# Optimization experiments

Hardware: AMD Instinct MI355X
Metric: run time of the kernel (lower is better)

## Reference

```python
import jax, jax.numpy as jnp
import numpy as np

# --- static mask-construction config (mirrors FlexAttnFunc.init_mask args) ---
B = 1
L_F, L_H, L_W = 8, 20, 36      # latent_shape[2:]
A_F, A_H, A_W = 8, 1, 1        # action_shape[2:]
PATCH = (1, 2, 2)
CHUNK = 1
PAD = 176
WINDOW = 6
DIM, HEADS, DHEAD = 1536, 12, 128
EPS = 1e-5


def _make_ids():
    lf, lh, lw = L_F // PATCH[0], L_H // PATCH[1], L_W // PATCH[2]
    lat_seq = np.repeat(np.arange(B), lf * lh * lw)
    act_seq = np.repeat(np.arange(B), A_F * A_H * A_W)
    seq = np.concatenate([lat_seq, lat_seq, act_seq, act_seq])
    lat_fr = np.broadcast_to(np.arange(L_F)[None, :, None, None], (B, L_F, lh, lw)).reshape(-1)
    act_fr = np.broadcast_to(np.arange(A_F)[None, :, None, None], (B, A_F, A_H, A_W)).reshape(-1)
    fr = np.concatenate([lat_fr // CHUNK * 2] * 2 + [act_fr // CHUNK * 2 + 1] * 2)
    nz = np.concatenate([np.zeros_like(lat_fr), np.ones_like(lat_fr),
                         np.zeros_like(act_fr), np.ones_like(act_fr)])
    pad = np.full(PAD, -1, dtype=np.int64)
    return (np.concatenate([seq, pad]).astype(np.int32),
            np.concatenate([fr, pad]).astype(np.int32),
            np.concatenate([nz, pad]).astype(np.int32))


def setup_inputs() -> dict:
    key = jax.random.key(0)
    ks = jax.random.split(key, 8)
    seq, fr, nz = _make_ids()
    S = seq.shape[0]  # 3072
    sd = 0.02
    return {
        'x': jax.random.normal(ks[0], (1, S, DIM), jnp.float32),
        'Wq': jax.random.normal(ks[1], (DIM, DIM), jnp.float32) * sd,
        'bq': jnp.zeros((DIM,), jnp.float32),
        'Wk': jax.random.normal(ks[2], (DIM, DIM), jnp.float32) * sd,
        'bk': jnp.zeros((DIM,), jnp.float32),
        'Wv': jax.random.normal(ks[3], (DIM, DIM), jnp.float32) * sd,
        'bv': jnp.zeros((DIM,), jnp.float32),
        'gq': 1.0 + jax.random.normal(ks[4], (DIM,), jnp.float32) * sd,
        'gk': 1.0 + jax.random.normal(ks[5], (DIM,), jnp.float32) * sd,
        'Wo': jax.random.normal(ks[6], (DIM, DIM), jnp.float32) * sd,
        'bo': jnp.zeros((DIM,), jnp.float32),
        'seq_ids': jnp.asarray(seq),
        'frame_ids': jnp.asarray(fr),
        'noise_ids': jnp.asarray(nz),
        'window_size': WINDOW,
    }


def _rms(u, g):
    # torch.nn.RMSNorm over last dim (size heads*dim_head), elementwise affine
    return u * jax.lax.rsqrt(jnp.mean(u * u, axis=-1, keepdims=True) + EPS) * g


def _mask(seq_ids, frame_ids, noise_ids, window_size):
    sq, sk = seq_ids[:, None], seq_ids[None, :]
    fq, fk = frame_ids[:, None], frame_ids[None, :]
    nq, nk = noise_ids[:, None], noise_ids[None, :]
    seq_ok = (sq == sk) & (sq >= 0) & (sk >= 0)
    c2c = (nq == 1) & (nk == 1) & (fk <= fq)      # clean->clean, block causal incl self
    n2c = (nq == 0) & (nk == 1) & (fk < fq)       # noise->clean, causal excl self
    n2n = (nq == 0) & (nk == 0) & (fk == fq)      # noise->noise, same frame only
    win = jnp.abs(fq - fk) <= window_size
    return (c2c | n2c | n2n) & seq_ok & win


def reference(x, Wq, bq, Wk, bk, Wv, bv, gq, gk, Wo, bo,
              seq_ids, frame_ids, noise_ids, window_size):
    S = x.shape[1]
    q = _rms(x @ Wq + bq, gq)[0].reshape(S, HEADS, DHEAD)
    k = _rms(x @ Wk + bk, gk)[0].reshape(S, HEADS, DHEAD)
    v = (x @ Wv + bv)[0].reshape(S, HEADS, DHEAD)
    mask = _mask(seq_ids, frame_ids, noise_ids, window_size)  # [S,S] bool
    scores = jnp.einsum('qhd,khd->hqk', q, k) * (DHEAD ** -0.5)
    scores = jnp.where(mask[None], scores, jnp.float32(-1e9))
    attn = jax.nn.softmax(scores, axis=-1)
    o = jnp.einsum('hqk,khd->qhd', attn, v)
    # zero out padded (fully-masked) query rows
    o = o * (seq_ids >= 0).astype(o.dtype)[:, None, None]
    y = o.reshape(1, S, HEADS * DHEAD) @ Wo + bo
    return y
```

## Files before the change

kernel.cpp:

```cpp
#include <hip/hip_runtime.h>
#include <hip/hip_bf16.h>
#include <stdint.h>

typedef __bf16 bf16x8 __attribute__((ext_vector_type(8)));
typedef float f32x4 __attribute__((ext_vector_type(4)));

__device__ __forceinline__ unsigned short f2bf(float f) {
  union { float f; unsigned int u; } v; v.f = f;
  unsigned int u = v.u;
  unsigned int r = (u + 0x7fffu + ((u >> 16) & 1u)) >> 16;
  return (unsigned short)r;
}
__device__ __forceinline__ float bf2f(unsigned short s) {
  union { unsigned int u; float f; } v; v.u = ((unsigned int)s) << 16; return v.f;
}

__global__ __launch_bounds__(256) void setup(
    const float* __restrict__ x,
    const float* __restrict__ Wq, const float* __restrict__ Wk,
    const float* __restrict__ Wv, const float* __restrict__ Wo,
    const int* __restrict__ seq, const int* __restrict__ fr,
    const int* __restrict__ nz, const int* __restrict__ wsz,
    unsigned short* __restrict__ x_bf, unsigned short* __restrict__ wt,
    unsigned long long* __restrict__ tbm, unsigned char* __restrict__ mb,
    float* __restrict__ ssq, int S) {
  __shared__ __align__(16) unsigned char smu[16384];
  int b = blockIdx.x, tid = threadIdx.x;
  if (b < 1152) {
    int base = b * 1024 + tid;
    for (int j = 0; j < 4; j++) {
      int i = base + j * 256;
      float4 v = ((const float4*)x)[i];
      ushort4 o;
      o.x = f2bf(v.x); o.y = f2bf(v.y); o.z = f2bf(v.z); o.w = f2bf(v.w);
      ((ushort4*)x_bf)[i] = o;
    }
  } else if (b < 3456) {
    int id = b - 1152;
    int z = id / 576, rem = id % 576;
    int kx = rem % 24, ny = rem / 24;
    const float* W = z == 0 ? Wq : (z == 1 ? Wk : (z == 2 ? Wv : Wo));
    unsigned short (*t)[65] = (unsigned short(*)[65])smu;
    int k0 = kx * 64, n0 = ny * 64;
    const int N = 1536, K = 1536;
    for (int i = 0; i < 16; i++) {
      int e = tid + i * 256;
      int r = e >> 6, c = e & 63;
      t[r][c] = f2bf(W[(size_t)(k0 + r) * N + n0 + c]);
    }
    __syncthreads();
    for (int i = 0; i < 16; i++) {
      int e = tid + i * 256;
      int r = e >> 6, c = e & 63;
      wt[(size_t)(z * 1536 + n0 + r) * K + k0 + c] = t[c][r];
    }
  } else if (b == 3456) {
    int* ks_ = (int*)smu;
    unsigned int* tm_ = (unsigned int*)(smu + 12288);
    int W = wsz[0];
    for (int i = tid; i < S; i += 256) {
      int sq = seq[i];
      ks_[i] = (sq < 0) ? 0 : ((1 << 9) | ((nz[i] & 1) << 8) | (fr[i] & 15) | (sq << 10));
    }
    for (int i = tid; i < 6144; i += 256) ssq[i] = 0.f;
    __syncthreads();
    for (int t = tid; t < S / 32; t += 256) {
      unsigned int m = 0;
      for (int j = 0; j < 32; j++) {
        int a = ks_[t * 32 + j];
        if (a & (1 << 9)) m |= (a & (1 << 8)) ? (1u << (16 + (a & 15))) : (1u << (a & 15));
      }
      tm_[t] = m;
    }
    __syncthreads();
    for (int qg = tid; qg < S / 16; qg += 256) {
      unsigned int allowed = 0;
      for (int j = 0; j < 16; j++) {
        int a = ks_[qg * 16 + j];
        if (!(a & (1 << 9))) continue;
        int fq = a & 15, nq = (a >> 8) & 1;
        int lo = fq - W; if (lo < 0) lo = 0;
        unsigned int lom = ~((1u << lo) - 1);
        if (nq) allowed |= (((1u << (fq + 1)) - 1) & lom) << 16;
        else    allowed |= ((((1u << fq) - 1) & lom) << 16) | (1u << fq);
      }
      unsigned long long b0 = 0, b1 = 0;
      for (int t = 0; t < 96; t++)
        if (tm_[t] & allowed) { if (t < 64) b0 |= 1ull << t; else b1 |= 1ull << (t - 64); }
      tbm[qg * 2] = b0; tbm[qg * 2 + 1] = b1;
    }
  } else {
    int qg = b - 3457;
    int* ks_ = (int*)smu;
    int W = wsz[0];
    for (int i = tid; i < S; i += 256) {
      int sq = seq[i];
      ks_[i] = (sq < 0) ? 0 : ((1 << 9) | ((nz[i] & 1) << 8) | (fr[i] & 15) | (sq << 10));
    }
    __syncthreads();
    int wave = tid >> 6, lane = tid & 63, quad = lane >> 4, l16 = lane & 15;
    int aq[4];
    for (int r = 0; r < 4; r++) aq[r] = ks_[qg * 16 + quad * 4 + r];
    for (int t = wave; t < 96; t += 4) {
      int ak[2] = { ks_[t * 32 + l16], ks_[t * 32 + 16 + l16] };
      unsigned int byte = 0;
      for (int nt = 0; nt < 2; nt++) {
        int a = ak[nt];
        int kfr = a & 15, knz = (a >> 8) & 1, kvb = (a >> 9) & 1, ksq = a >> 10;
        for (int r = 0; r < 4; r++) {
          int bq_ = aq[r];
          int qfr = bq_ & 15, qnz = (bq_ >> 8) & 1, qvb = (bq_ >> 9) & 1, qsq = bq_ >> 10;
          bool ok  = qvb && kvb && (qsq == ksq);
          bool c2c = qnz && knz && (kfr <= qfr);
          bool n2c = !qnz && knz && (kfr < qfr);
          bool n2n = !qnz && !knz && (kfr == qfr);
          int df = qfr - kfr; df = df < 0 ? -df : df;
          if ((c2c || n2c || n2n) && ok && (df <= W)) byte |= 1u << (nt * 4 + r);
        }
      }
      mb[((size_t)qg * 96 + t) * 64 + lane] = (unsigned char)byte;
    }
  }
}

__global__ __launch_bounds__(512) void gemm_qkv(
    const unsigned short* __restrict__ A, const unsigned short* __restrict__ Bt,
    const float* __restrict__ bq, const float* __restrict__ bk, const float* __restrict__ bv,
    const float* __restrict__ gq, const float* __restrict__ gk,
    unsigned short* __restrict__ qt, unsigned short* __restrict__ ktb,
    unsigned short* __restrict__ vtb, float* __restrict__ ssq, int S) {
  __shared__ __align__(16) unsigned short smem[65536];
  int tid = threadIdx.x, wid = tid >> 6, lane = tid & 63;
  int quad = lane >> 4, l16 = lane & 15;
  int m0 = blockIdx.x * 256, n0 = blockIdx.y * 256;
  int wm = (wid >> 2) * 128;
  int wn = (wid & 3) * 64;
  int lr = lane >> 3;
  int lsw = ((lane & 7) ^ lr) * 8;
  int sx = l16 & 7;

  f32x4 acc[8][4] = {};

#define STAGEQ(t_, q_) do { \
    if ((t_) < 24) { \
      int b_ = (t_) & 1; \
      int k0_ = (t_) * 64; \
      unsigned short* ldsb = ((q_) < 2) ? (smem + b_ * 16384) : (smem + 32768 + b_ * 16384); \
      const unsigned short* gsrc = ((q_) < 2) ? A : Bt; \
      int rbase = ((q_) < 2) ? m0 : n0; \
      int lo8_ = ((q_) & 1) * 8; \
      for (int c_ = 0; c_ < 2; c_++) { \
        int chunk = lo8_ + c_ * 16 + wid; \
        const unsigned short* src = gsrc + (size_t)(rbase + chunk * 8 + lr) * 1536 + k0_ + lsw; \
        __builtin_amdgcn_global_load_lds( \
            (const __attribute__((address_space(1))) unsigned int*)src, \
            (__attribute__((address_space(3))) unsigned int*)(ldsb + chunk * 512 + lane * 8), 16, 0, 0); \
      } \
    } } while (0)

  STAGEQ(0, 0); STAGEQ(0, 1); STAGEQ(0, 2); STAGEQ(0, 3);
  STAGEQ(1, 0);
  asm volatile("s_waitcnt vmcnt(2)" ::: "memory");
  __builtin_amdgcn_s_barrier();
  __builtin_amdgcn_sched_barrier(0);

#define PHASE(p) do { \
    constexpr int q_ = (p) & 3; \
    constexpr int tb_ = (p) >> 2; \
    constexpr int k8_ = (q_ >> 1) * 4; \
    constexpr int mi0_ = (q_ & 1) * 4; \
    unsigned short* Ab = smem + tb_ * 16384; \
    unsigned short* Bb = smem + 32768 + tb_ * 16384; \
    int so_ = ((k8_ + quad) ^ sx) << 3; \
    if constexpr ((q_ & 1) == 0) { \
      for (int nj = 0; nj < 4; nj++) \
        bfr[nj] = *(const bf16x8*)&Bb[(wn + nj * 16 + l16) * 64 + so_]; \
    } \
    bf16x8 af[4]; \
    for (int ii = 0; ii < 4; ii++) \
      af[ii] = *(const bf16x8*)&Ab[(wm + (mi0_ + ii) * 16 + l16) * 64 + so_]; \
    STAGEQ(2 * i + kStT[p], kStQ[p]); \
    __builtin_amdgcn_sched_barrier(0); \
    __builtin_amdgcn_s_barrier(); \
    asm volatile("s_waitcnt lgkmcnt(0)" ::: "memory"); \
    __builtin_amdgcn_sched_barrier(0); \
    __builtin_amdgcn_s_setprio(1); \
    for (int ii = 0; ii < 4; ii++) \
      for (int nj = 0; nj < 4; nj++) \
        acc[mi0_ + ii][nj] = __builtin_amdgcn_mfma_f32_16x16x32_bf16(af[ii], bfr[nj], acc[mi0_ + ii][nj], 0, 0, 0); \
    __builtin_amdgcn_s_setprio(0); \
    if constexpr (q_ == 3) { asm volatile("s_waitcnt vmcnt(2)" ::: "memory"); } \
    __builtin_amdgcn_s_barrier(); \
    __builtin_amdgcn_sched_barrier(0); \
  } while (0)

  constexpr int kStT[8] = {1, 1, 1, 2, 2, 2, 2, 3};
  constexpr int kStQ[8] = {1, 2, 3, 0, 1, 2, 3, 0};

  for (int i = 0; i < 12; i++) {
    bf16x8 bfr[4];
    PHASE(0); PHASE(1); PHASE(2); PHASE(3);
    PHASE(4); PHASE(5); PHASE(6); PHASE(7);
  }
#undef PHASE
#undef STAGEQ

  int region = (n0 >= 3072) ? 2 : (n0 >= 1536 ? 1 : 0);
  int cbase = n0 - region * 1536;
  int hh0 = cbase >> 7;
  unsigned short* Cs = smem;
  if (region < 2) {
    const float* bias = region == 0 ? bq : bk;
    float* ssqp = ssq + region * 3072;
    float ss[8][4] = {};
    for (int nj = 0; nj < 4; nj++) {
      int col = wn + nj * 16 + l16;
      float b = bias[cbase + col];
      float G = (region == 1) ? gq[cbase + col] * gk[cbase + col] : 1.0f;
      for (int mi = 0; mi < 8; mi++)
        for (int r = 0; r < 4; r++) {
          float v = acc[mi][nj][r] + b;
          ss[mi][r] += v * v;
          Cs[(wm + mi * 16 + quad * 4 + r) * 256 + col] = f2bf(v * G);
        }
    }
    for (int mi = 0; mi < 8; mi++)
      for (int r = 0; r < 4; r++) {
        float v = ss[mi][r];
        for (int o = 1; o < 16; o <<= 1) v += __shfl_xor(v, o);
        if (l16 == 0)
          atomicAdd(&ssqp[m0 + wm + mi * 16 + quad * 4 + r], v);
      }
    __syncthreads();
    unsigned short* outb = (region == 0 ? qt : ktb);
    for (int p = 0; p < 16; p++) {
      int o = p * 4096 + tid * 8;
      int row = o >> 8, col = o & 255;
      size_t dst = (size_t)(hh0 + (col >> 7)) * 393216 + (size_t)(m0 + row) * 128 + (col & 127);
      *(uint4*)&outb[dst] = *(const uint4*)&Cs[o];
    }
  } else {
    for (int nj = 0; nj < 4; nj++) {
      int col = wn + nj * 16 + l16;
      float b = bv[cbase + col];
      int c8 = l16 * 8;
      for (int mi = 0; mi < 8; mi++)
        for (int r = 0; r < 4; r++) {
          int sp = wm + mi * 16 + quad * 4 + r;
          Cs[col * 256 + (sp ^ c8)] = f2bf(acc[mi][nj][r] + b);
        }
    }
    __syncthreads();
    for (int hh = 0; hh < 2; hh++) {
      unsigned short* outp = vtb + ((size_t)(hh0 + hh) * 96 + (m0 >> 5)) * 4096;
      for (int p = 0; p < 8; p++) {
        int o = p * 4096 + tid * 8;
        int tile = o >> 12, rem = o & 4095;
        int dd = rem >> 5, s31 = rem & 31;
        int laddr = (hh * 128 + dd) * 256 + ((tile * 32 + s31) ^ ((dd & 15) * 8));
        *(uint4*)&outp[o] = *(const uint4*)&Cs[laddr];
      }
    }
  }
}

__global__ __launch_bounds__(256) void gemm_wo(
    const unsigned short* __restrict__ A, const unsigned short* __restrict__ Bt,
    const float* __restrict__ bias, float* __restrict__ C, int M, int N, int K) {
  __shared__ __align__(16) unsigned short As[128 * 64];
  __shared__ __align__(16) unsigned short Bs[64 * 64];
  int tid = threadIdx.x, wave = tid >> 6, lane = tid & 63;
  int quad = lane >> 4, l16 = lane & 15;
  int m0 = blockIdx.x * 128, n0 = blockIdx.y * 64;
  int wm = (wave & 1) * 64, wn = (wave >> 1) * 32;
  int lr = lane >> 3;
  int lc = ((lane & 7) ^ lr) * 8;
  int sx = l16 & 7;
  f32x4 acc[4][2] = {};
  for (int k0 = 0; k0 < K; k0 += 64) {
    for (int c = 0; c < 4; c++) {
      int chunk = wave * 4 + c;
      int row = chunk * 8 + lr;
      const unsigned short* ga = &A[(size_t)(m0 + row) * K + k0 + lc];
      __builtin_amdgcn_global_load_lds(
          (const __attribute__((address_space(1))) unsigned int*)ga,
          (__attribute__((address_space(3))) unsigned int*)(As + chunk * 512), 16, 0, 0);
    }
    for (int c = 0; c < 2; c++) {
      int chunk = wave * 2 + c;
      int row = chunk * 8 + lr;
      const unsigned short* gb = &Bt[(size_t)(n0 + row) * K + k0 + lc];
      __builtin_amdgcn_global_load_lds(
          (const __attribute__((address_space(1))) unsigned int*)gb,
          (__attribute__((address_space(3))) unsigned int*)(Bs + chunk * 512), 16, 0, 0);
    }
    __syncthreads();
    for (int kk = 0; kk < 64; kk += 32) {
      int k8 = kk >> 3;
      int sw = ((k8 + quad) ^ sx) << 3;
      bf16x8 af[4], bfr[2];
      for (int i = 0; i < 4; i++)
        af[i] = *(const bf16x8*)&As[(wm + i * 16 + l16) * 64 + sw];
      for (int j = 0; j < 2; j++)
        bfr[j] = *(const bf16x8*)&Bs[(wn + j * 16 + l16) * 64 + sw];
      for (int i = 0; i < 4; i++)
        for (int j = 0; j < 2; j++)
          acc[i][j] = __builtin_amdgcn_mfma_f32_16x16x32_bf16(af[i], bfr[j], acc[i][j], 0, 0, 0);
    }
    __syncthreads();
  }
  for (int j = 0; j < 2; j++) {
    int col = n0 + wn + j * 16 + l16;
    float b = bias[col];
    for (int i = 0; i < 4; i++)
      for (int r = 0; r < 4; r++)
        C[(size_t)(m0 + wm + i * 16 + quad * 4 + r) * N + col] = acc[i][j][r] + b;
  }
}

__global__ __launch_bounds__(256) void attn(
    const unsigned short* __restrict__ qt,
    const unsigned short* __restrict__ kt,
    const unsigned short* __restrict__ vt,
    const unsigned char* __restrict__ mb,
    const unsigned long long* __restrict__ tbm,
    const float* __restrict__ ssq,
    unsigned short* __restrict__ op0b, unsigned short* __restrict__ op1b,
    float* __restrict__ lp, int S) {
  const int h = blockIdx.x;
  const int qb64 = blockIdx.y;
  const int split = blockIdx.z;
  int tid = threadIdx.x, wave = tid >> 6, lane = tid & 63;
  int quad = lane >> 4, l16 = lane & 15;
  const float scale = 0.088388347648318447f;

  __shared__ __align__(16) unsigned short pshare[4][16][40];

  int qg = qb64 * 4 + wave;
  unsigned long long bm0 = tbm[qg * 2], bm1 = tbm[qg * 2 + 1];

  const unsigned short* kth = kt + (size_t)h * 96 * 4096;
  const unsigned short* vth = vt + (size_t)h * 96 * 4096;
  const unsigned char* mbq = mb + (size_t)qg * 96 * 64;

  bf16x8 qf[4];
  {
    const unsigned short* qp = qt + ((size_t)(h * 192 + qg) * 16 + l16) * 128 + quad * 8;
    for (int ks = 0; ks < 4; ks++) qf[ks] = *(const bf16x8*)&qp[ks * 32];
  }
  float qs[4];
  for (int r = 0; r < 4; r++) {
    int row = qb64 * 64 + wave * 16 + quad * 4 + r;
    qs[r] = rsqrtf(ssq[row] * (1.0f / 1536.0f) + 1e-5f) * scale;
  }
  const float* ssk = ssq + 3072;

  f32x4 oacc[8] = {};
  f32x4 lacc = {};
  const __bf16 onebf = (__bf16)1.0f;
  const bf16x8 ones = {onebf, onebf, onebf, onebf, onebf, onebf, onebf, onebf};

#define POP(dst) do { \
    if (bm0) { dst = __builtin_ctzll(bm0); bm0 &= bm0 - 1; } \
    else if (bm1) { dst = 64 + __builtin_ctzll(bm1); bm1 &= bm1 - 1; } \
    else dst = -1; } while (0)

  int t, dsc;
  if (split) POP(dsc);
  POP(t);

  while (t >= 0) {
    const unsigned short* kp = kth + (size_t)t * 4096 + (size_t)l16 * 128 + quad * 8;
    bf16x8 kf[2][4];
    for (int nt = 0; nt < 2; nt++)
      for (int ks = 0; ks < 4; ks++)
        kf[nt][ks] = *(const bf16x8*)&kp[nt * 2048 + ks * 32];
    unsigned int mbyte = mbq[t * 64 + lane];
    float kss0 = ssk[t * 32 + l16], kss1 = ssk[t * 32 + 16 + l16];

    f32x4 sacc[2] = {};
    for (int nt = 0; nt < 2; nt++)
      for (int ks = 0; ks < 4; ks++)
        sacc[nt] = __builtin_amdgcn_mfma_f32_16x16x32_bf16(qf[ks], kf[nt][ks], sacc[nt], 0, 0, 0);

    const unsigned short* vp = vth + (size_t)t * 4096 + (size_t)l16 * 32 + quad * 8;
    bf16x8 vf[8];
    for (int d = 0; d < 8; d++)
      vf[d] = *(const bf16x8*)&vp[d * 512];

    float ksc0 = rsqrtf(kss0 * (1.0f / 1536.0f) + 1e-5f);
    float ksc1 = rsqrtf(kss1 * (1.0f / 1536.0f) + 1e-5f);
    for (int nt = 0; nt < 2; nt++) {
      float kscv = nt == 0 ? ksc0 : ksc1;
      for (int r = 0; r < 4; r++) {
        float e = __expf(sacc[nt][r] * (qs[r] * kscv) - 16.0f);
        float p = ((mbyte >> (nt * 4 + r)) & 1) ? e : 0.0f;
        pshare[wave][quad * 4 + r][nt * 16 + l16] = f2bf(p);
      }
    }
    __asm__ __volatile__("s_waitcnt lgkmcnt(0)" ::: "memory");
    bf16x8 pf = *(const bf16x8*)&pshare[wave][l16][quad * 8];
    for (int d = 0; d < 8; d++)
      oacc[d] = __builtin_amdgcn_mfma_f32_16x16x32_bf16(pf, vf[d], oacc[d], 0, 0, 0);
    lacc = __builtin_amdgcn_mfma_f32_16x16x32_bf16(pf, ones, lacc, 0, 0, 0);

    POP(dsc);
    POP(t);
  }
#undef POP

  unsigned short* po = split ? op1b : op0b;
  for (int r = 0; r < 4; r++) {
    int q = qb64 * 64 + wave * 16 + quad * 4 + r;
    float inv = (lacc[r] > 0.f) ? 1.0f / lacc[r] : 0.0f;
    for (int d = 0; d < 8; d++)
      po[((size_t)h * S + q) * 128 + d * 16 + l16] = f2bf(oacc[d][r] * inv);
    if (l16 == 0)
      lp[((size_t)split * 12 + h) * S + q] = lacc[r];
  }
}

__global__ __launch_bounds__(256) void combine(const unsigned short* __restrict__ op0b,
                                               const unsigned short* __restrict__ op1b,
                                               const float* __restrict__ lp,
                                               const int* __restrict__ seq,
                                               unsigned short* __restrict__ ob, int S) {
  int e4 = blockIdx.x * 256 + threadIdx.x;
  int idx = e4 * 4;
  int per_h = S * 128;
  int h = idx / per_h;
  int rem = idx - h * per_h;
  int q = rem >> 7, dd = rem & 127;
  float l0 = lp[(size_t)h * S + q], l1 = lp[(size_t)(12 + h) * S + q];
  float tot = l0 + l1;
  float ok = (seq[q] >= 0 && tot > 0.f) ? 1.0f / tot : 0.0f;
  float w0 = l0 * ok, w1 = l1 * ok;
  ushort4 a = ((const ushort4*)op0b)[e4];
  ushort4 b = ((const ushort4*)op1b)[e4];
  ushort4 o;
  o.x = f2bf(bf2f(a.x) * w0 + bf2f(b.x) * w1);
  o.y = f2bf(bf2f(a.y) * w0 + bf2f(b.y) * w1);
  o.z = f2bf(bf2f(a.z) * w0 + bf2f(b.z) * w1);
  o.w = f2bf(bf2f(a.w) * w0 + bf2f(b.w) * w1);
  *(ushort4*)&ob[(size_t)q * 1536 + h * 128 + dd] = o;
}

extern "C" void kernel_launch(void* const* d_in, const int* in_sizes, int n_in,
                              void* d_out, int out_size, void* d_ws, size_t ws_size,
                              hipStream_t stream) {
  const float* x  = (const float*)d_in[0];
  const float* Wq = (const float*)d_in[1];
  const float* bq = (const float*)d_in[2];
  const float* Wk = (const float*)d_in[3];
  const float* bk = (const float*)d_in[4];
  const float* Wv = (const float*)d_in[5];
  const float* bv = (const float*)d_in[6];
  const float* gq = (const float*)d_in[7];
  const float* gk = (const float*)d_in[8];
  const float* Wo = (const float*)d_in[9];
  const float* bo = (const float*)d_in[10];
  const int* seq  = (const int*)d_in[11];
  const int* fr   = (const int*)d_in[12];
  const int* nz   = (const int*)d_in[13];
  const int* wsz  = (const int*)d_in[14];
  float* out = (float*)d_out;
  const int S = in_sizes[11];
  const int D = 1536;

  char* ws = (char*)d_ws;
  size_t off = 0;
  unsigned short* x_bf = (unsigned short*)(ws + off); off += (size_t)S * D * 2;
  unsigned short* wt   = (unsigned short*)(ws + off); off += (size_t)4 * D * D * 2;
  unsigned short* qt   = (unsigned short*)(ws + off); off += (size_t)S * D * 2;
  unsigned short* ktb  = (unsigned short*)(ws + off); off += (size_t)S * D * 2;
  unsigned short* vtb  = (unsigned short*)(ws + off); off += (size_t)S * D * 2;
  unsigned short* o_bf = (unsigned short*)(ws + off); off += (size_t)S * D * 2;
  unsigned short* op0b = (unsigned short*)(ws + off); off += (size_t)S * D * 2;
  unsigned short* op1b = (unsigned short*)(ws + off); off += (size_t)S * D * 2;
  unsigned long long* tbm = (unsigned long long*)(ws + off); off += (size_t)(S / 16) * 16;
  unsigned char*  mbuf = (unsigned char*)(ws + off);  off += (size_t)(S / 16) * 96 * 64;
  float*          lp   = (float*)(ws + off);          off += (size_t)2 * 12 * S * 4;
  float*          ssq  = (float*)(ws + off);          off += (size_t)2 * 3072 * 4;

  dim3 blk(256);
  setup<<<dim3(3649), blk, 0, stream>>>(x, Wq, Wk, Wv, Wo, seq, fr, nz, wsz,
                                        x_bf, wt, tbm, mbuf, ssq, S);
  gemm_qkv<<<dim3(S / 256, 3 * D / 256), dim3(512), 0, stream>>>(x_bf, wt, bq, bk, bv, gq, gk,
                                                                 qt, ktb, vtb, ssq, S);
  attn<<<dim3(D / 128, S / 64, 2), blk, 0, stream>>>(qt, ktb, vtb, mbuf, tbm, ssq,
                                                     op0b, op1b, lp, S);
  combine<<<dim3(12 * S * 128 / 4 / 256), blk, 0, stream>>>(op0b, op1b, lp, seq, o_bf, S);
  gemm_wo<<<dim3(S / 128, D / 64), blk, 0, stream>>>(o_bf, wt + (size_t)3 * D * D,
                                                     bo, out, S, D, D);
}
```

Before: 318.8 us.

## Double-buffer K/V tile loads in attention loop with MFMA priority boosts

Restructures the sparse-tile attention loop into a two-stage software pipeline that prefetches the next tile's K, V, mask byte and key norms into a second register set while the current tile computes. Sched barriers keep the loads issued ahead of the MFMA work, and s_setprio raises wave priority around MFMA bursts. This aims to hide global load latency behind compute. The cost is roughly double the register use for K/V fragments, which may lower occupancy or cause spills.

```diff
diff --git a/kernel.cpp b/kernel.cpp
--- a/kernel.cpp
+++ b/kernel.cpp
@@ -365,49 +365,71 @@
     else if (bm1) { dst = 64 + __builtin_ctzll(bm1); bm1 &= bm1 - 1; } \
     else dst = -1; } while (0)
 
+#define LOADT(K_, V_, M_, S0_, S1_, t_) do { \
+    const unsigned short* kp_ = kth + (size_t)(t_) * 4096 + (size_t)l16 * 128 + quad * 8; \
+    for (int nt = 0; nt < 2; nt++) \
+      for (int ks = 0; ks < 4; ks++) \
+        K_[nt][ks] = *(const bf16x8*)&kp_[nt * 2048 + ks * 32]; \
+    const unsigned short* vp_ = vth + (size_t)(t_) * 4096 + (size_t)l16 * 32 + quad * 8; \
+    for (int d = 0; d < 8; d++) \
+      V_[d] = *(const bf16x8*)&vp_[d * 512]; \
+    M_ = mbq[(t_) * 64 + lane]; \
+    S0_ = ssk[(t_) * 32 + l16]; S1_ = ssk[(t_) * 32 + 16 + l16]; \
+  } while (0)
+
+#define COMPUTE(K_, V_, M_, S0_, S1_) do { \
+    f32x4 sacc[2] = {}; \
+    __builtin_amdgcn_s_setprio(1); \
+    for (int nt = 0; nt < 2; nt++) \
+      for (int ks = 0; ks < 4; ks++) \
+        sacc[nt] = __builtin_amdgcn_mfma_f32_16x16x32_bf16(qf[ks], K_[nt][ks], sacc[nt], 0, 0, 0); \
+    __builtin_amdgcn_s_setprio(0); \
+    float ksc0_ = rsqrtf(S0_ * (1.0f / 1536.0f) + 1e-5f); \
+    float ksc1_ = rsqrtf(S1_ * (1.0f / 1536.0f) + 1e-5f); \
+    for (int nt = 0; nt < 2; nt++) { \
+      float kscv_ = nt == 0 ? ksc0_ : ksc1_; \
+      for (int r = 0; r < 4; r++) { \
+        float e_ = __expf(sacc[nt][r] * (qs[r] * kscv_) - 16.0f); \
+        float p_ = ((M_ >> (nt * 4 + r)) & 1) ? e_ : 0.0f; \
+        pshare[wave][quad * 4 + r][nt * 16 + l16] = f2bf(p_); \
+      } \
+    } \
+    __asm__ __volatile__("s_waitcnt lgkmcnt(0)" ::: "memory"); \
+    bf16x8 pf_ = *(const bf16x8*)&pshare[wave][l16][quad * 8]; \
+    __builtin_amdgcn_s_setprio(1); \
+    for (int d = 0; d < 8; d++) \
+      oacc[d] = __builtin_amdgcn_mfma_f32_16x16x32_bf16(pf_, V_[d], oacc[d], 0, 0, 0); \
+    lacc = __builtin_amdgcn_mfma_f32_16x16x32_bf16(pf_, ones, lacc, 0, 0, 0); \
+    __builtin_amdgcn_s_setprio(0); \
+  } while (0)
+
+  bf16x8 kfA[2][4], vfA[8], kfB[2][4], vfB[8];
+  unsigned int mbA = 0, mbB = 0;
+  float sA0 = 0.f, sA1 = 0.f, sB0 = 0.f, sB1 = 0.f;
+
   int t, dsc;
   if (split) POP(dsc);
   POP(t);
+  if (t >= 0) LOADT(kfA, vfA, mbA, sA0, sA1, t);
 
   while (t >= 0) {
-    const unsigned short* kp = kth + (size_t)t * 4096 + (size_t)l16 * 128 + quad * 8;
-    bf16x8 kf[2][4];
-    for (int nt = 0; nt < 2; nt++)
-      for (int ks = 0; ks < 4; ks++)
-        kf[nt][ks] = *(const bf16x8*)&kp[nt * 2048 + ks * 32];
-    unsigned int mbyte = mbq[t * 64 + lane];
-    float kss0 = ssk[t * 32 + l16], kss1 = ssk[t * 32 + 16 + l16];
-
-    f32x4 sacc[2] = {};
-    for (int nt = 0; nt < 2; nt++)
-      for (int ks = 0; ks < 4; ks++)
-        sacc[nt] = __builtin_amdgcn_mfma_f32_16x16x32_bf16(qf[ks], kf[nt][ks], sacc[nt], 0, 0, 0);
-
-    const unsigned short* vp = vth + (size_t)t * 4096 + (size_t)l16 * 32 + quad * 8;
-    bf16x8 vf[8];
-    for (int d = 0; d < 8; d++)
-      vf[d] = *(const bf16x8*)&vp[d * 512];
-
-    float ksc0 = rsqrtf(kss0 * (1.0f / 1536.0f) + 1e-5f);
-    float ksc1 = rsqrtf(kss1 * (1.0f / 1536.0f) + 1e-5f);
-    for (int nt = 0; nt < 2; nt++) {
-      float kscv = nt == 0 ? ksc0 : ksc1;
-      for (int r = 0; r < 4; r++) {
-        float e = __expf(sacc[nt][r] * (qs[r] * kscv) - 16.0f);
-        float p = ((mbyte >> (nt * 4 + r)) & 1) ? e : 0.0f;
-        pshare[wave][quad * 4 + r][nt * 16 + l16] = f2bf(p);
-      }
-    }
-    __asm__ __volatile__("s_waitcnt lgkmcnt(0)" ::: "memory");
-    bf16x8 pf = *(const bf16x8*)&pshare[wave][l16][quad * 8];
-    for (int d = 0; d < 8; d++)
-      oacc[d] = __builtin_amdgcn_mfma_f32_16x16x32_bf16(pf, vf[d], oacc[d], 0, 0, 0);
-    lacc = __builtin_amdgcn_mfma_f32_16x16x32_bf16(pf, ones, lacc, 0, 0, 0);
-
-    POP(dsc);
-    POP(t);
+    int tn;
+    POP(dsc); POP(tn);
+    if (tn >= 0) LOADT(kfB, vfB, mbB, sB0, sB1, tn);
+    __builtin_amdgcn_sched_barrier(0);
+    COMPUTE(kfA, vfA, mbA, sA0, sA1);
+    t = tn;
+    if (t < 0) break;
+
+    POP(dsc); POP(tn);
+    if (tn >= 0) LOADT(kfA, vfA, mbA, sA0, sA1, tn);
+    __builtin_amdgcn_sched_barrier(0);
+    COMPUTE(kfB, vfB, mbB, sB0, sB1);
+    t = tn;
   }
 #undef POP
+#undef LOADT
+#undef COMPUTE
 
   unsigned short* po = split ? op1b : op0b;
   for (int r = 0; r < 4; r++) {
```

After: 316.1 us. About the same (-0.8%).
